# Performance work log

Measured on AMD Instinct MI355X. Metric: run time of the kernel, lower is better.

## Reference

```python
import jax, jax.numpy as jnp
import numpy as np

B, T, LD, PD, W, NL = 2048, 256, 32, 8, 64, 3
TH, CH = LD * 2, W * 2  # token/channel mixing hidden dims (expansion=2)


def setup_inputs() -> dict:
    key = jax.random.key(0)
    ks = jax.random.split(key, 12)
    n = lambda k, s, sc=0.02: jax.random.normal(k, s, jnp.float32) * sc
    return {
        "phys": jax.random.normal(ks[0], (B, T, PD), jnp.float32),
        "latents": jax.random.uniform(ks[1], (B, LD), jnp.float32),
        "pos_emb": n(ks[2], (1, LD, W)),
        "tokW": n(ks[3], (1, W)), "tokb": jnp.zeros((W,), jnp.float32),
        "physW1": n(ks[4], (PD, W)), "physb1": jnp.zeros((W,), jnp.float32),
        "physW2": n(ks[5], (W, W)), "physb2": jnp.zeros((W,), jnp.float32),
        "tn_g": jnp.ones((NL, W), jnp.float32), "tn_b": jnp.zeros((NL, W), jnp.float32),
        "tiW": n(ks[6], (NL, LD, TH)), "tib": jnp.zeros((NL, TH), jnp.float32),
        "toW": n(ks[7], (NL, TH, LD)), "tob": jnp.zeros((NL, LD), jnp.float32),
        "cn_g": jnp.ones((NL, W), jnp.float32), "cn_b": jnp.zeros((NL, W), jnp.float32),
        "ciW": n(ks[8], (NL, W, CH)), "cib": jnp.zeros((NL, CH), jnp.float32),
        "coW": n(ks[9], (NL, CH, W)), "cob": jnp.zeros((NL, W), jnp.float32),
        "hn_g": jnp.ones((W,), jnp.float32), "hn_b": jnp.zeros((W,), jnp.float32),
        "headW": n(ks[10], (W, 1), 0.0002),  # 0.02 init * 0.01 scaling from torch
        "headb": jnp.zeros((1,), jnp.float32),
    }


def _ln(x, g, b):
    m = jnp.mean(x, -1, keepdims=True)
    v = jnp.mean((x - m) ** 2, -1, keepdims=True)
    return (x - m) * jax.lax.rsqrt(v + 1e-5) * g + b


def reference(phys, latents, pos_emb, tokW, tokb, physW1, physb1, physW2, physb2,
              tn_g, tn_b, tiW, tib, toW, tob, cn_g, cn_b, ciW, cib, coW, cob,
              hn_g, hn_b, headW, headb):
    gelu = lambda x: jax.nn.gelu(x, approximate=False)  # torch nn.GELU default (exact)

    def step(current, phys_t):
        # token_projection of current[..., None]: Linear(1, W)
        tokens = current[:, :, None] * tokW[0] + tokb  # [B, LD, W]
        p = gelu(phys_t @ physW1 + physb1) @ physW2 + physb2  # [B, W]
        tokens = tokens + p[:, None, :] + pos_emb
        for i in range(NL):
            # token mixing: LN over width, mix across latent tokens
            mt = jnp.swapaxes(_ln(tokens, tn_g[i], tn_b[i]), 1, 2)  # [B, W, LD]
            mt = gelu(mt @ tiW[i] + tib[i]) @ toW[i] + tob[i]       # [B, W, LD]
            tokens = tokens + jnp.swapaxes(mt, 1, 2)
            # channel mixing over width
            mc = _ln(tokens, cn_g[i], cn_b[i])
            tokens = tokens + (gelu(mc @ ciW[i] + cib[i]) @ coW[i] + cob[i])
        delta = (_ln(tokens, hn_g, hn_b) @ headW + headb)[..., 0]  # [B, LD]
        new = jnp.clip(current + delta, 0.0, 1.0)
        return new, new

    _, outs = jax.lax.scan(step, latents, jnp.swapaxes(phys, 0, 1))  # [T, B, LD]
    return jnp.swapaxes(outs, 0, 1)  # [B, T, LD]
```

## Files before the change

### kernel.cpp

```cpp
#include <hip/hip_runtime.h>
#include <math.h>


namespace {
constexpr int Tt = 256, NL = 3;

typedef float    f32x4 __attribute__((ext_vector_type(4)));
typedef _Float16 half2 __attribute__((ext_vector_type(2)));
typedef _Float16 h16x4 __attribute__((ext_vector_type(4)));
typedef _Float16 h16x8 __attribute__((ext_vector_type(8)));

#define MFMA16(a, b, c) __builtin_amdgcn_mfma_f32_16x16x32_f16((a), (b), (c), 0, 0, 0)

__device__ __forceinline__ half2 h2c(float v) { return (half2)((_Float16)v); }
__device__ __forceinline__ f32x4 f4s(float v) { return (f32x4)v; }
__device__ __forceinline__ half2 pkrtz(float a, float b) {
    return __builtin_bit_cast(half2, __builtin_amdgcn_cvt_pkrtz(a, b));
}
__device__ __forceinline__ void st4h(short* p, half2 a, half2 b) {
    uint2 v;
    v.x = __builtin_bit_cast(unsigned int, a);
    v.y = __builtin_bit_cast(unsigned int, b);
    *(uint2*)p = v;
}
__device__ __forceinline__ half2 gelu_pk(half2 x) {
    half2 tc = __builtin_elementwise_min(__builtin_elementwise_max(x, h2c(-3.0f)), h2c(3.0f));
    half2 s = (tc * tc) * h2c(0.125f);
    half2 p = s * h2c(0.1455169f) + h2c(-0.446340f);
    p = s * p + h2c(0.604927f);
    p = s * p + h2c(-0.529702f);
    p = s * p + h2c(0.3989423f);
    return x * (h2c(0.5f) + tc * p);
}
__device__ __forceinline__ float gelu_f(float x) {
    float tc = fminf(fmaxf(x, -3.f), 3.f);
    float s = tc * tc;
    float p = fmaf(s, 3.55266e-5f, -8.71758e-4f);
    p = fmaf(s, p, 9.45198e-3f);
    p = fmaf(s, p, -6.62128e-2f);
    p = fmaf(s, p, 0.3989423f);
    return x * fmaf(tc, p, 0.5f);
}
__device__ __forceinline__ float rowsum16(float x) {
    x += __builtin_bit_cast(float, __builtin_amdgcn_update_dpp(0, __builtin_bit_cast(int, x), 0x121, 0xf, 0xf, false));
    x += __builtin_bit_cast(float, __builtin_amdgcn_update_dpp(0, __builtin_bit_cast(int, x), 0x122, 0xf, 0xf, false));
    x += __builtin_bit_cast(float, __builtin_amdgcn_update_dpp(0, __builtin_bit_cast(int, x), 0x124, 0xf, 0xf, false));
    x += __builtin_bit_cast(float, __builtin_amdgcn_update_dpp(0, __builtin_bit_cast(int, x), 0x128, 0xf, 0xf, false));
    return x;
}

__device__ __forceinline__ short f2h(float x) {
    return __builtin_bit_cast(short, (_Float16)x);
}

__global__ void lno_prep(const float* __restrict__ tiW, const float* __restrict__ toW,
                         const float* __restrict__ ciW, const float* __restrict__ coW,
                         const float* __restrict__ physW2, short* __restrict__ wsf) {
    int id = blockIdx.x * 256 + threadIdx.x;
    if (id < 6144) {
        int j = id & 7, lane = (id >> 3) & 63, g = id >> 9;
        int il = g >> 2, u = g & 3;
        int m = u * 16 + (lane & 15), k = (lane >> 4) * 8 + j;
        wsf[id] = f2h(tiW[il * 2048 + k * 64 + m]);
    } else if (id < 12288) {
        int t = id - 6144;
        int j = t & 7, lane = (t >> 3) & 63, g = t >> 9;
        int il = g >> 2, mt2 = (g >> 1) & 1, ks = g & 1;
        int m = mt2 * 16 + (lane & 15), k = ks * 32 + (lane >> 4) * 8 + j;
        wsf[id] = f2h(toW[il * 2048 + k * 32 + m]);
    } else if (id < 36864) {
        int t = id - 12288;
        int j = t & 7, lane = (t >> 3) & 63, g = t >> 9;
        int il = g >> 4, mtc = (g >> 1) & 7, ks = g & 1;
        int m = mtc * 16 + (lane & 15), k = ks * 32 + (lane >> 4) * 8 + j;
        wsf[id] = f2h(ciW[il * 8192 + k * 128 + m]);
    } else if (id < 61440) {
        int t = id - 36864;
        int j = t & 7, lane = (t >> 3) & 63, g = t >> 9;
        int il = g >> 4, nt = (g >> 2) & 3, ks = g & 3;
        int n = nt * 16 + (lane & 15), k = ks * 32 + (lane >> 4) * 8 + j;
        wsf[id] = f2h(coW[il * 8192 + k * 64 + n]);
    } else if (id < 65536) {
        int t = id - 61440;
        int w = t >> 6, k = t & 63;
        ((float*)(wsf + 61440))[t] = physW2[k * 64 + w];
    }
}

__global__ void lno_phys(const float* __restrict__ phys, const float* __restrict__ physW1,
                         const float* __restrict__ physb1, const float* __restrict__ physW2,
                         const float* __restrict__ physb2, short* __restrict__ pout) {
    __shared__ float hsh[4][64];
    const int lane = threadIdx.x & 63, wv = threadIdx.x >> 6;
    const size_t bt = (size_t)blockIdx.x * 4 + wv;
    const float* pt = phys + bt * 8;
    float4 px0 = *(const float4*)pt, px1 = *(const float4*)(pt + 4);
    float a = physb1[lane];
    a = fmaf(px0.x, physW1[0 * 64 + lane], a);
    a = fmaf(px0.y, physW1[1 * 64 + lane], a);
    a = fmaf(px0.z, physW1[2 * 64 + lane], a);
    a = fmaf(px0.w, physW1[3 * 64 + lane], a);
    a = fmaf(px1.x, physW1[4 * 64 + lane], a);
    a = fmaf(px1.y, physW1[5 * 64 + lane], a);
    a = fmaf(px1.z, physW1[6 * 64 + lane], a);
    a = fmaf(px1.w, physW1[7 * 64 + lane], a);
    hsh[wv][lane] = gelu_f(a);
    float acc = physb2[lane];
#pragma unroll
    for (int k = 0; k < 64; ++k) acc = fmaf(hsh[wv][k], physW2[k * 64 + lane], acc);
    pout[bt * 64 + (lane & 15) * 4 + (lane >> 4)] = f2h(acc);
}

__global__ __launch_bounds__(512, 2) void lno_scan(
    const float* __restrict__ latents, const float* __restrict__ pos_emb,
    const float* __restrict__ tokW,    const float* __restrict__ tokb,
    const float* __restrict__ tn_g,    const float* __restrict__ tn_b,
    const float* __restrict__ tib,     const float* __restrict__ tob,
    const float* __restrict__ cn_g,    const float* __restrict__ cn_b,
    const float* __restrict__ cib,     const float* __restrict__ cob,
    const float* __restrict__ hn_g,    const float* __restrict__ hn_b,
    const float* __restrict__ headW,   const float* __restrict__ headb,
    const short* __restrict__ wsf,     const short* pbuf, float* out)
{
    __shared__ __align__(16) short wAll[61440];
    __shared__ __align__(16) short scr[8][2048];
    __shared__ __align__(16) float biasL[1632];

    const int tid = threadIdx.x, lane = tid & 63, wv = tid >> 6;
    const int q = lane >> 4, c = lane & 15;
    const int b = blockIdx.x * 8 + wv;
    short* sc = scr[wv];

    const short* tiL = wAll;
    const short* toL = wAll + 6144;
    const short* ciL = wAll + 12288;
    const short* coL = wAll + 36864;

    {
        const unsigned int* src = (const unsigned int*)wsf;
#pragma unroll
        for (int i = 0; i < 15; ++i) {
            const int cid = wv * 15 + i;
            __builtin_amdgcn_global_load_lds(src + cid * 256 + lane * 4,
                                             (unsigned int*)&wAll[cid * 512], 16, 0, 0);
        }
    }
    for (int i = tid; i < 192; i += 512) {
        biasL[i] = tib[i];
        biasL[672 + i]  = tn_g[i];
        biasL[864 + i]  = tn_b[i];
        biasL[1056 + i] = cn_g[i];
        biasL[1248 + i] = cn_b[i];
        biasL[1440 + i] = cob[i];
    }
    for (int i = tid; i < 96;  i += 512) biasL[192 + i] = tob[i];
    for (int i = tid; i < 384; i += 512) biasL[288 + i] = cib[i];

    float tokw_r[4], tokb_r[4], gh_r[4];
#pragma unroll
    for (int nt = 0; nt < 4; ++nt) {
        tokw_r[nt] = tokW[nt * 16 + c];
        tokb_r[nt] = tokb[nt * 16 + c];
        gh_r[nt]   = hn_g[nt * 16 + c] * headW[nt * 16 + c];
    }
    float bhp = 0.f;
#pragma unroll
    for (int nt = 0; nt < 4; ++nt) bhp = fmaf(hn_b[nt * 16 + c], headW[nt * 16 + c], bhp);
    const float bh = rowsum16(bhp) + headb[0];

    f32x4 pe4[2][4];
#pragma unroll
    for (int mt = 0; mt < 2; ++mt)
#pragma unroll
        for (int nt = 0; nt < 4; ++nt)
#pragma unroll
            for (int r = 0; r < 4; ++r)
                pe4[mt][nt][r] = pos_emb[(mt * 16 + q * 4 + r) * 64 + nt * 16 + c];

    f32x4 cur8[2];
#pragma unroll
    for (int mt = 0; mt < 2; ++mt)
        cur8[mt] = *(const f32x4*)(latents + b * 32 + mt * 16 + q * 4);

    f32x4 tok[2][4];

    __syncthreads();

    auto stats = [&](f32x4 (&mean)[2], f32x4 (&rsig)[2]) {
#pragma unroll
        for (int mt = 0; mt < 2; ++mt) {
            f32x4 s4 = (tok[mt][0] + tok[mt][1]) + (tok[mt][2] + tok[mt][3]);
            f32x4 q4 = tok[mt][0] * tok[mt][0];
            q4 = __builtin_elementwise_fma(tok[mt][1], tok[mt][1], q4);
            q4 = __builtin_elementwise_fma(tok[mt][2], tok[mt][2], q4);
            q4 = __builtin_elementwise_fma(tok[mt][3], tok[mt][3], q4);
#pragma unroll
            for (int r = 0; r < 4; ++r) {
                float s = rowsum16(s4[r]);
                float qq = rowsum16(q4[r]);
                float m = s * 0.015625f;
                float v = fmaf(-m, m, qq * 0.015625f);
                mean[mt][r] = m;
                rsig[mt][r] = __builtin_amdgcn_rsqf(v + 1e-5f);
            }
        }
    };

    const short* pb = pbuf + (size_t)b * Tt * 64 + c * 4;
    h16x4 pvc = *(const h16x4*)pb;

#pragma unroll 1
    for (int t = 0; t < Tt; ++t) {
        const h16x4 pv = pvc;
        if (t + 1 < Tt) pvc = *(const h16x4*)(pb + (t + 1) * 64);

#pragma unroll
        for (int nt = 0; nt < 4; ++nt) {
            const f32x4 bp = f4s(tokb_r[nt] + (float)pv[nt]);
            const f32x4 tw = f4s(tokw_r[nt]);
#pragma unroll
            for (int mt = 0; mt < 2; ++mt)
                tok[mt][nt] = __builtin_elementwise_fma(cur8[mt], tw, pe4[mt][nt] + bp);
        }

#pragma unroll
        for (int il = 0; il < NL; ++il) {
            f32x4 mean[2], rsig[2];
            stats(mean, rsig);
            float tng[4], tnb[4];
#pragma unroll
            for (int nt = 0; nt < 4; ++nt) {
                tng[nt] = biasL[672 + il * 64 + nt * 16 + c];
                tnb[nt] = biasL[864 + il * 64 + nt * 16 + c];
            }
#pragma unroll
            for (int mt = 0; mt < 2; ++mt)
#pragma unroll
                for (int nt = 0; nt < 4; ++nt) {
                    f32x4 y = __builtin_elementwise_fma((tok[mt][nt] - mean[mt]) * rsig[mt],
                                                        f4s(tng[nt]), f4s(tnb[nt]));
                    st4h(&sc[(nt * 64 + (mt * 2 + (q >> 1)) * 16 + c) * 8 + (q & 1) * 4],
                         pkrtz(y[0], y[1]), pkrtz(y[2], y[3]));
                }
            h16x8 yfrag[4];
#pragma unroll
            for (int nt = 0; nt < 4; ++nt) yfrag[nt] = *(const h16x8*)&sc[(nt * 64 + lane) * 8];

#pragma unroll
            for (int mt = 0; mt < 2; ++mt) {
                const f32x4 tb = *(const f32x4*)&biasL[192 + il * 32 + mt * 16 + q * 4];
#pragma unroll
                for (int nt = 0; nt < 4; ++nt) tok[mt][nt] += tb;
            }
#pragma unroll
            for (int h = 0; h < 2; ++h) {
#pragma unroll
                for (int uu = 0; uu < 2; ++uu) {
                    const int u = h * 2 + uu;
                    const h16x8 a1 = *(const h16x8*)(tiL + ((il * 4 + u) * 64 + lane) * 8);
                    const f32x4 bi = *(const f32x4*)&biasL[il * 64 + u * 16 + q * 4];
#pragma unroll
                    for (int nt = 0; nt < 4; ++nt) {
                        f32x4 acc = MFMA16(a1, yfrag[nt], bi);
                        st4h(&sc[(nt * 64 + (uu * 2 + (q >> 1)) * 16 + c) * 8 + (q & 1) * 4],
                             gelu_pk(pkrtz(acc[0], acc[1])), gelu_pk(pkrtz(acc[2], acc[3])));
                    }
                }
                h16x8 hf[4];
#pragma unroll
                for (int nt = 0; nt < 4; ++nt) hf[nt] = *(const h16x8*)&sc[(nt * 64 + lane) * 8];
#pragma unroll
                for (int mt = 0; mt < 2; ++mt) {
                    const h16x8 a2 = *(const h16x8*)(toL + ((il * 4 + mt * 2 + h) * 64 + lane) * 8);
#pragma unroll
                    for (int nt = 0; nt < 4; ++nt) tok[mt][nt] = MFMA16(a2, hf[nt], tok[mt][nt]);
                }
            }

            stats(mean, rsig);
            float cng[4], cnb[4];
#pragma unroll
            for (int nt = 0; nt < 4; ++nt) {
                cng[nt] = biasL[1056 + il * 64 + nt * 16 + c];
                cnb[nt] = biasL[1248 + il * 64 + nt * 16 + c];
            }
#pragma unroll
            for (int mt = 0; mt < 2; ++mt)
#pragma unroll
                for (int nt = 0; nt < 4; ++nt) {
                    f32x4 v4 = __builtin_elementwise_fma((tok[mt][nt] - mean[mt]) * rsig[mt],
                                                         f4s(cng[nt]), f4s(cnb[nt]));
#pragma unroll
                    for (int r = 0; r < 4; ++r)
                        sc[(mt * 2 + (nt >> 1)) * 512 +
                           (q * 2 + (c >> 3) + 16 * r + 8 * (nt & 1)) * 8 + (c & 7)] = f2h(v4[r]);
                }
            h16x8 b3[4];
            {
                const int lp = ((c >> 2) * 2 + (q & 1)) + 8 * ((c & 3) * 2 + (q >> 1));
#pragma unroll
                for (int F = 0; F < 4; ++F) b3[F] = *(const h16x8*)&sc[F * 512 + lp * 8];
            }
#pragma unroll
            for (int nt = 0; nt < 4; ++nt) {
                const f32x4 cv = f4s(biasL[1440 + il * 64 + nt * 16 + c]);
#pragma unroll
                for (int mt = 0; mt < 2; ++mt) tok[mt][nt] += cv;
            }

#pragma unroll
            for (int hh = 0; hh < 2; ++hh) {
#pragma unroll
                for (int mm = 0; mm < 4; ++mm) {
                    const int mtc = hh * 4 + mm;
                    const h16x8 a30 = *(const h16x8*)(ciL + il * 8192 + (mtc * 2 + 0) * 512 + lane * 8);
                    const h16x8 a31 = *(const h16x8*)(ciL + il * 8192 + (mtc * 2 + 1) * 512 + lane * 8);
                    const f32x4 bi3 = *(const f32x4*)&biasL[288 + il * 128 + mtc * 16 + q * 4];
#pragma unroll
                    for (int ntl = 0; ntl < 2; ++ntl) {
                        f32x4 acc = MFMA16(a30, b3[ntl * 2 + 0], bi3);
                        acc = MFMA16(a31, b3[ntl * 2 + 1], acc);
                        st4h(&sc[((ntl * 2 + ((mtc >> 1) & 1)) * 64 +
                                  ((mtc & 1) * 2 + (q >> 1)) * 16 + c) * 8 + (q & 1) * 4],
                             gelu_pk(pkrtz(acc[0], acc[1])), gelu_pk(pkrtz(acc[2], acc[3])));
                    }
                }
                h16x8 a4[2][2];
#pragma unroll
                for (int mt = 0; mt < 2; ++mt)
#pragma unroll
                    for (int kk = 0; kk < 2; ++kk)
                        a4[mt][kk] = *(const h16x8*)&sc[((mt * 2 + kk) * 64 + lane) * 8];
#pragma unroll
                for (int nt = 0; nt < 4; ++nt) {
                    const h16x8 b40 = *(const h16x8*)(coL + il * 8192 + (nt * 4 + hh * 2 + 0) * 512 + lane * 8);
                    const h16x8 b41 = *(const h16x8*)(coL + il * 8192 + (nt * 4 + hh * 2 + 1) * 512 + lane * 8);
#pragma unroll
                    for (int mt = 0; mt < 2; ++mt) {
                        tok[mt][nt] = MFMA16(a4[mt][0], b40, tok[mt][nt]);
                        tok[mt][nt] = MFMA16(a4[mt][1], b41, tok[mt][nt]);
                    }
                }
            }
        }

        {
            f32x4 mean[2], rsig[2];
            stats(mean, rsig);
#pragma unroll
            for (int mt = 0; mt < 2; ++mt) {
                f32x4 l4 = (tok[mt][0] - mean[mt]) * f4s(gh_r[0]);
                l4 = __builtin_elementwise_fma(tok[mt][1] - mean[mt], f4s(gh_r[1]), l4);
                l4 = __builtin_elementwise_fma(tok[mt][2] - mean[mt], f4s(gh_r[2]), l4);
                l4 = __builtin_elementwise_fma(tok[mt][3] - mean[mt], f4s(gh_r[3]), l4);
                f32x4 ls;
#pragma unroll
                for (int r = 0; r < 4; ++r) ls[r] = rowsum16(l4[r]);
                f32x4 nv = cur8[mt] + __builtin_elementwise_fma(rsig[mt], ls, f4s(bh));
                nv = __builtin_elementwise_min(__builtin_elementwise_max(nv, f4s(0.f)), f4s(1.f));
                cur8[mt] = nv;
            }
            if (c == 0) {
                float* op = out + ((size_t)b * Tt + t) * 32 + q * 4;
                *(f32x4*)(op) = cur8[0];
                *(f32x4*)(op + 16) = cur8[1];
            }
        }
    }
}
}

extern "C" void kernel_launch(void* const* d_in, const int* in_sizes, int n_in,
                              void* d_out, int out_size, void* d_ws, size_t ws_size,
                              hipStream_t stream) {
    (void)in_sizes; (void)n_in; (void)ws_size; (void)out_size;
    const float* phys    = (const float*)d_in[0];
    const float* latents = (const float*)d_in[1];
    const float* pos_emb = (const float*)d_in[2];
    const float* tokW    = (const float*)d_in[3];
    const float* tokb    = (const float*)d_in[4];
    const float* physW1  = (const float*)d_in[5];
    const float* physb1  = (const float*)d_in[6];
    const float* physW2  = (const float*)d_in[7];
    const float* physb2  = (const float*)d_in[8];
    const float* tn_g    = (const float*)d_in[9];
    const float* tn_b    = (const float*)d_in[10];
    const float* tiW     = (const float*)d_in[11];
    const float* tib     = (const float*)d_in[12];
    const float* toW     = (const float*)d_in[13];
    const float* tob     = (const float*)d_in[14];
    const float* cn_g    = (const float*)d_in[15];
    const float* cn_b    = (const float*)d_in[16];
    const float* ciW     = (const float*)d_in[17];
    const float* cib     = (const float*)d_in[18];
    const float* coW     = (const float*)d_in[19];
    const float* cob     = (const float*)d_in[20];
    const float* hn_g    = (const float*)d_in[21];
    const float* hn_b    = (const float*)d_in[22];
    const float* headW   = (const float*)d_in[23];
    const float* headb   = (const float*)d_in[24];

    lno_prep<<<dim3(256), dim3(256), 0, stream>>>(tiW, toW, ciW, coW, physW2, (short*)d_ws);
    lno_phys<<<dim3(131072), dim3(256), 0, stream>>>(phys, physW1, physb1, physW2, physb2,
                                                     (short*)d_out);
    lno_scan<<<dim3(256), dim3(512), 0, stream>>>(
        latents, pos_emb, tokW, tokb, tn_g, tn_b, tib, tob,
        cn_g, cn_b, cib, cob, hn_g, hn_b, headW, headb,
        (const short*)d_ws, (const short*)d_out, (float*)d_out);
}
```

Measured before the change: 6.166 ms.

## Process two batch sequences per wavefront to add ILP in scan kernel

Each wavefront now carries two independent batch rows through the 256-step recurrence, so the block shrinks to 4 waves of 256 threads while keeping 8 rows per block. The two independent MFMA and LayerNorm chains are interleaved to hide latency on the serial time dependency, and weight A-fragments are reused across both rows. In exchange register pressure roughly doubles, the layer loop is no longer unrolled, and there are half as many waves per CU to hide stalls.

```diff
diff --git a/kernel.cpp b/kernel.cpp
--- a/kernel.cpp
+++ b/kernel.cpp
@@ -111,7 +111,7 @@
     pout[bt * 64 + (lane & 15) * 4 + (lane >> 4)] = f2h(acc);
 }
 
-__global__ __launch_bounds__(512, 2) void lno_scan(
+__global__ __launch_bounds__(256, 1) void lno_scan(
     const float* __restrict__ latents, const float* __restrict__ pos_emb,
     const float* __restrict__ tokW,    const float* __restrict__ tokb,
     const float* __restrict__ tn_g,    const float* __restrict__ tn_b,
@@ -123,29 +123,29 @@
     const short* __restrict__ wsf,     const short* pbuf, float* out)
 {
     __shared__ __align__(16) short wAll[61440];
-    __shared__ __align__(16) short scr[8][2048];
+    __shared__ __align__(16) short scr[4][4096];
     __shared__ __align__(16) float biasL[1632];
 
     const int tid = threadIdx.x, lane = tid & 63, wv = tid >> 6;
     const int q = lane >> 4, c = lane & 15;
-    const int b = blockIdx.x * 8 + wv;
-    short* sc = scr[wv];
+    const int bb = (blockIdx.x * 4 + wv) * 2;
 
     const short* tiL = wAll;
     const short* toL = wAll + 6144;
     const short* ciL = wAll + 12288;
     const short* coL = wAll + 36864;
+    short* const scp[2] = { &scr[wv][0], &scr[wv][2048] };
 
     {
         const unsigned int* src = (const unsigned int*)wsf;
 #pragma unroll
-        for (int i = 0; i < 15; ++i) {
-            const int cid = wv * 15 + i;
+        for (int i = 0; i < 30; ++i) {
+            const int cid = wv * 30 + i;
             __builtin_amdgcn_global_load_lds(src + cid * 256 + lane * 4,
                                              (unsigned int*)&wAll[cid * 512], 16, 0, 0);
         }
     }
-    for (int i = tid; i < 192; i += 512) {
+    for (int i = tid; i < 192; i += 256) {
         biasL[i] = tib[i];
         biasL[672 + i]  = tn_g[i];
         biasL[864 + i]  = tn_b[i];
@@ -153,8 +153,8 @@
         biasL[1248 + i] = cn_b[i];
         biasL[1440 + i] = cob[i];
     }
-    for (int i = tid; i < 96;  i += 512) biasL[192 + i] = tob[i];
-    for (int i = tid; i < 384; i += 512) biasL[288 + i] = cib[i];
+    for (int i = tid; i < 96;  i += 256) biasL[192 + i] = tob[i];
+    for (int i = tid; i < 384; i += 256) biasL[288 + i] = cib[i];
 
     float tokw_r[4], tokb_r[4], gh_r[4];
 #pragma unroll
@@ -177,28 +177,30 @@
             for (int r = 0; r < 4; ++r)
                 pe4[mt][nt][r] = pos_emb[(mt * 16 + q * 4 + r) * 64 + nt * 16 + c];
 
-    f32x4 cur8[2];
-#pragma unroll
-    for (int mt = 0; mt < 2; ++mt)
-        cur8[mt] = *(const f32x4*)(latents + b * 32 + mt * 16 + q * 4);
-
-    f32x4 tok[2][4];
+    f32x4 cur8[2][2];
+#pragma unroll
+    for (int s = 0; s < 2; ++s)
+#pragma unroll
+        for (int mt = 0; mt < 2; ++mt)
+            cur8[s][mt] = *(const f32x4*)(latents + (bb + s) * 32 + mt * 16 + q * 4);
+
+    f32x4 tok[2][2][4];
 
     __syncthreads();
 
-    auto stats = [&](f32x4 (&mean)[2], f32x4 (&rsig)[2]) {
+    auto stats1 = [&](const f32x4 (&tk)[2][4], f32x4 (&mean)[2], f32x4 (&rsig)[2]) {
 #pragma unroll
         for (int mt = 0; mt < 2; ++mt) {
-            f32x4 s4 = (tok[mt][0] + tok[mt][1]) + (tok[mt][2] + tok[mt][3]);
-            f32x4 q4 = tok[mt][0] * tok[mt][0];
-            q4 = __builtin_elementwise_fma(tok[mt][1], tok[mt][1], q4);
-            q4 = __builtin_elementwise_fma(tok[mt][2], tok[mt][2], q4);
-            q4 = __builtin_elementwise_fma(tok[mt][3], tok[mt][3], q4);
+            f32x4 s4 = (tk[mt][0] + tk[mt][1]) + (tk[mt][2] + tk[mt][3]);
+            f32x4 q4 = tk[mt][0] * tk[mt][0];
+            q4 = __builtin_elementwise_fma(tk[mt][1], tk[mt][1], q4);
+            q4 = __builtin_elementwise_fma(tk[mt][2], tk[mt][2], q4);
+            q4 = __builtin_elementwise_fma(tk[mt][3], tk[mt][3], q4);
 #pragma unroll
             for (int r = 0; r < 4; ++r) {
-                float s = rowsum16(s4[r]);
+                float ss = rowsum16(s4[r]);
                 float qq = rowsum16(q4[r]);
-                float m = s * 0.015625f;
+                float m = ss * 0.015625f;
                 float v = fmaf(-m, m, qq * 0.015625f);
                 mean[mt][r] = m;
                 rsig[mt][r] = __builtin_amdgcn_rsqf(v + 1e-5f);
@@ -206,27 +208,35 @@
         }
     };
 
-    const short* pb = pbuf + (size_t)b * Tt * 64 + c * 4;
-    h16x4 pvc = *(const h16x4*)pb;
+    const short* pb0 = pbuf + (size_t)(bb + 0) * Tt * 64 + c * 4;
+    const short* pb1 = pbuf + (size_t)(bb + 1) * Tt * 64 + c * 4;
+    h16x4 pvc0 = *(const h16x4*)pb0;
+    h16x4 pvc1 = *(const h16x4*)pb1;
 
 #pragma unroll 1
     for (int t = 0; t < Tt; ++t) {
-        const h16x4 pv = pvc;
-        if (t + 1 < Tt) pvc = *(const h16x4*)(pb + (t + 1) * 64);
-
-#pragma unroll
-        for (int nt = 0; nt < 4; ++nt) {
-            const f32x4 bp = f4s(tokb_r[nt] + (float)pv[nt]);
-            const f32x4 tw = f4s(tokw_r[nt]);
-#pragma unroll
-            for (int mt = 0; mt < 2; ++mt)
-                tok[mt][nt] = __builtin_elementwise_fma(cur8[mt], tw, pe4[mt][nt] + bp);
+        const h16x4 pv[2] = { pvc0, pvc1 };
+        if (t + 1 < Tt) {
+            pvc0 = *(const h16x4*)(pb0 + (t + 1) * 64);
+            pvc1 = *(const h16x4*)(pb1 + (t + 1) * 64);
         }
 
 #pragma unroll
+        for (int s = 0; s < 2; ++s)
+#pragma unroll
+            for (int nt = 0; nt < 4; ++nt) {
+                const f32x4 bp = f4s(tokb_r[nt] + (float)pv[s][nt]);
+                const f32x4 tw = f4s(tokw_r[nt]);
+#pragma unroll
+                for (int mt = 0; mt < 2; ++mt)
+                    tok[s][mt][nt] = __builtin_elementwise_fma(cur8[s][mt], tw, pe4[mt][nt] + bp);
+            }
+
+#pragma unroll 1
         for (int il = 0; il < NL; ++il) {
-            f32x4 mean[2], rsig[2];
-            stats(mean, rsig);
+            f32x4 mean[2][2], rsig[2][2];
+#pragma unroll
+            for (int s = 0; s < 2; ++s) stats1(tok[s], mean[s], rsig[s]);
             float tng[4], tnb[4];
 #pragma unroll
             for (int nt = 0; nt < 4; ++nt) {
@@ -234,50 +244,66 @@
                 tnb[nt] = biasL[864 + il * 64 + nt * 16 + c];
             }
 #pragma unroll
-            for (int mt = 0; mt < 2; ++mt)
-#pragma unroll
-                for (int nt = 0; nt < 4; ++nt) {
-                    f32x4 y = __builtin_elementwise_fma((tok[mt][nt] - mean[mt]) * rsig[mt],
-                                                        f4s(tng[nt]), f4s(tnb[nt]));
-                    st4h(&sc[(nt * 64 + (mt * 2 + (q >> 1)) * 16 + c) * 8 + (q & 1) * 4],
-                         pkrtz(y[0], y[1]), pkrtz(y[2], y[3]));
-                }
-            h16x8 yfrag[4];
-#pragma unroll
-            for (int nt = 0; nt < 4; ++nt) yfrag[nt] = *(const h16x8*)&sc[(nt * 64 + lane) * 8];
+            for (int s = 0; s < 2; ++s)
+#pragma unroll
+                for (int mt = 0; mt < 2; ++mt)
+#pragma unroll
+                    for (int nt = 0; nt < 4; ++nt) {
+                        f32x4 y = __builtin_elementwise_fma((tok[s][mt][nt] - mean[s][mt]) * rsig[s][mt],
+                                                            f4s(tng[nt]), f4s(tnb[nt]));
+                        st4h(&scp[s][(nt * 64 + (mt * 2 + (q >> 1)) * 16 + c) * 8 + (q & 1) * 4],
+                             pkrtz(y[0], y[1]), pkrtz(y[2], y[3]));
+                    }
+            h16x8 yfrag[2][4];
+#pragma unroll
+            for (int s = 0; s < 2; ++s)
+#pragma unroll
+                for (int nt = 0; nt < 4; ++nt)
+                    yfrag[s][nt] = *(const h16x8*)&scp[s][(nt * 64 + lane) * 8];
 
 #pragma unroll
             for (int mt = 0; mt < 2; ++mt) {
                 const f32x4 tb = *(const f32x4*)&biasL[192 + il * 32 + mt * 16 + q * 4];
 #pragma unroll
-                for (int nt = 0; nt < 4; ++nt) tok[mt][nt] += tb;
+                for (int s = 0; s < 2; ++s)
+#pragma unroll
+                    for (int nt = 0; nt < 4; ++nt) tok[s][mt][nt] += tb;
             }
 #pragma unroll
             for (int h = 0; h < 2; ++h) {
 #pragma unroll
                 for (int uu = 0; uu < 2; ++uu) {
-                    const int u = h * 2 + uu;
-                    const h16x8 a1 = *(const h16x8*)(tiL + ((il * 4 + u) * 64 + lane) * 8);
-                    const f32x4 bi = *(const f32x4*)&biasL[il * 64 + u * 16 + q * 4];
-#pragma unroll
-                    for (int nt = 0; nt < 4; ++nt) {
-                        f32x4 acc = MFMA16(a1, yfrag[nt], bi);
-                        st4h(&sc[(nt * 64 + (uu * 2 + (q >> 1)) * 16 + c) * 8 + (q & 1) * 4],
-                             gelu_pk(pkrtz(acc[0], acc[1])), gelu_pk(pkrtz(acc[2], acc[3])));
-                    }
-                }
-                h16x8 hf[4];
-#pragma unroll
-                for (int nt = 0; nt < 4; ++nt) hf[nt] = *(const h16x8*)&sc[(nt * 64 + lane) * 8];
+                    const int uw = h * 2 + uu;
+                    const h16x8 a1 = *(const h16x8*)(tiL + ((il * 4 + uw) * 64 + lane) * 8);
+                    const f32x4 bi = *(const f32x4*)&biasL[il * 64 + uw * 16 + q * 4];
+#pragma unroll
+                    for (int s = 0; s < 2; ++s)
+#pragma unroll
+                        for (int nt = 0; nt < 4; ++nt) {
+                            f32x4 acc = MFMA16(a1, yfrag[s][nt], bi);
+                            st4h(&scp[s][(nt * 64 + (uu * 2 + (q >> 1)) * 16 + c) * 8 + (q & 1) * 4],
+                                 gelu_pk(pkrtz(acc[0], acc[1])), gelu_pk(pkrtz(acc[2], acc[3])));
+                        }
+                }
+                h16x8 hf[2][4];
+#pragma unroll
+                for (int s = 0; s < 2; ++s)
+#pragma unroll
+                    for (int nt = 0; nt < 4; ++nt)
+                        hf[s][nt] = *(const h16x8*)&scp[s][(nt * 64 + lane) * 8];
 #pragma unroll
                 for (int mt = 0; mt < 2; ++mt) {
                     const h16x8 a2 = *(const h16x8*)(toL + ((il * 4 + mt * 2 + h) * 64 + lane) * 8);
 #pragma unroll
-                    for (int nt = 0; nt < 4; ++nt) tok[mt][nt] = MFMA16(a2, hf[nt], tok[mt][nt]);
-                }
-            }
-
-            stats(mean, rsig);
+                    for (int s = 0; s < 2; ++s)
+#pragma unroll
+                        for (int nt = 0; nt < 4; ++nt)
+                            tok[s][mt][nt] = MFMA16(a2, hf[s][nt], tok[s][mt][nt]);
+                }
+            }
+
+#pragma unroll
+            for (int s = 0; s < 2; ++s) stats1(tok[s], mean[s], rsig[s]);
             float cng[4], cnb[4];
 #pragma unroll
             for (int nt = 0; nt < 4; ++nt) {
@@ -285,27 +311,34 @@
                 cnb[nt] = biasL[1248 + il * 64 + nt * 16 + c];
             }
 #pragma unroll
-            for (int mt = 0; mt < 2; ++mt)
-#pragma unroll
-                for (int nt = 0; nt < 4; ++nt) {
-                    f32x4 v4 = __builtin_elementwise_fma((tok[mt][nt] - mean[mt]) * rsig[mt],
-                                                         f4s(cng[nt]), f4s(cnb[nt]));
-#pragma unroll
-                    for (int r = 0; r < 4; ++r)
-                        sc[(mt * 2 + (nt >> 1)) * 512 +
-                           (q * 2 + (c >> 3) + 16 * r + 8 * (nt & 1)) * 8 + (c & 7)] = f2h(v4[r]);
-                }
-            h16x8 b3[4];
+            for (int s = 0; s < 2; ++s)
+#pragma unroll
+                for (int mt = 0; mt < 2; ++mt)
+#pragma unroll
+                    for (int nt = 0; nt < 4; ++nt) {
+                        f32x4 v4 = __builtin_elementwise_fma((tok[s][mt][nt] - mean[s][mt]) * rsig[s][mt],
+                                                             f4s(cng[nt]), f4s(cnb[nt]));
+#pragma unroll
+                        for (int r = 0; r < 4; ++r)
+                            scp[s][(mt * 2 + (nt >> 1)) * 512 +
+                                   (q * 2 + (c >> 3) + 16 * r + 8 * (nt & 1)) * 8 + (c & 7)] = f2h(v4[r]);
+                    }
+            h16x8 b3[2][4];
             {
                 const int lp = ((c >> 2) * 2 + (q & 1)) + 8 * ((c & 3) * 2 + (q >> 1));
 #pragma unroll
-                for (int F = 0; F < 4; ++F) b3[F] = *(const h16x8*)&sc[F * 512 + lp * 8];
+                for (int s = 0; s < 2; ++s)
+#pragma unroll
+                    for (int F = 0; F < 4; ++F)
+                        b3[s][F] = *(const h16x8*)&scp[s][F * 512 + lp * 8];
             }
 #pragma unroll
             for (int nt = 0; nt < 4; ++nt) {
                 const f32x4 cv = f4s(biasL[1440 + il * 64 + nt * 16 + c]);
 #pragma unroll
-                for (int mt = 0; mt < 2; ++mt) tok[mt][nt] += cv;
+                for (int s = 0; s < 2; ++s)
+#pragma unroll
+                    for (int mt = 0; mt < 2; ++mt) tok[s][mt][nt] += cv;
             }
 
 #pragma unroll
@@ -317,53 +350,65 @@
                     const h16x8 a31 = *(const h16x8*)(ciL + il * 8192 + (mtc * 2 + 1) * 512 + lane * 8);
                     const f32x4 bi3 = *(const f32x4*)&biasL[288 + il * 128 + mtc * 16 + q * 4];
 #pragma unroll
-                    for (int ntl = 0; ntl < 2; ++ntl) {
-                        f32x4 acc = MFMA16(a30, b3[ntl * 2 + 0], bi3);
-                        acc = MFMA16(a31, b3[ntl * 2 + 1], acc);
-                        st4h(&sc[((ntl * 2 + ((mtc >> 1) & 1)) * 64 +
-                                  ((mtc & 1) * 2 + (q >> 1)) * 16 + c) * 8 + (q & 1) * 4],
-                             gelu_pk(pkrtz(acc[0], acc[1])), gelu_pk(pkrtz(acc[2], acc[3])));
-                    }
-                }
-                h16x8 a4[2][2];
-#pragma unroll
-                for (int mt = 0; mt < 2; ++mt)
-#pragma unroll
-                    for (int kk = 0; kk < 2; ++kk)
-                        a4[mt][kk] = *(const h16x8*)&sc[((mt * 2 + kk) * 64 + lane) * 8];
+                    for (int s = 0; s < 2; ++s)
+#pragma unroll
+                        for (int ntl = 0; ntl < 2; ++ntl) {
+                            f32x4 acc = MFMA16(a30, b3[s][ntl * 2 + 0], bi3);
+                            acc = MFMA16(a31, b3[s][ntl * 2 + 1], acc);
+                            st4h(&scp[s][((ntl * 2 + ((mtc >> 1) & 1)) * 64 +
+                                          ((mtc & 1) * 2 + (q >> 1)) * 16 + c) * 8 + (q & 1) * 4],
+                                 gelu_pk(pkrtz(acc[0], acc[1])), gelu_pk(pkrtz(acc[2], acc[3])));
+                        }
+                }
+                h16x8 a4[2][2][2];
+#pragma unroll
+                for (int s = 0; s < 2; ++s)
+#pragma unroll
+                    for (int mt = 0; mt < 2; ++mt)
+#pragma unroll
+                        for (int kk = 0; kk < 2; ++kk)
+                            a4[s][mt][kk] = *(const h16x8*)&scp[s][((mt * 2 + kk) * 64 + lane) * 8];
 #pragma unroll
                 for (int nt = 0; nt < 4; ++nt) {
                     const h16x8 b40 = *(const h16x8*)(coL + il * 8192 + (nt * 4 + hh * 2 + 0) * 512 + lane * 8);
                     const h16x8 b41 = *(const h16x8*)(coL + il * 8192 + (nt * 4 + hh * 2 + 1) * 512 + lane * 8);
 #pragma unroll
-                    for (int mt = 0; mt < 2; ++mt) {
-                        tok[mt][nt] = MFMA16(a4[mt][0], b40, tok[mt][nt]);
-                        tok[mt][nt] = MFMA16(a4[mt][1], b41, tok[mt][nt]);
-                    }
+                    for (int s = 0; s < 2; ++s)
+#pragma unroll
+                        for (int mt = 0; mt < 2; ++mt) {
+                            tok[s][mt][nt] = MFMA16(a4[s][mt][0], b40, tok[s][mt][nt]);
+                            tok[s][mt][nt] = MFMA16(a4[s][mt][1], b41, tok[s][mt][nt]);
+                        }
                 }
             }
         }
 
         {
-            f32x4 mean[2], rsig[2];
-            stats(mean, rsig);
-#pragma unroll
-            for (int mt = 0; mt < 2; ++mt) {
-                f32x4 l4 = (tok[mt][0] - mean[mt]) * f4s(gh_r[0]);
-                l4 = __builtin_elementwise_fma(tok[mt][1] - mean[mt], f4s(gh_r[1]), l4);
-                l4 = __builtin_elementwise_fma(tok[mt][2] - mean[mt], f4s(gh_r[2]), l4);
-                l4 = __builtin_elementwise_fma(tok[mt][3] - mean[mt], f4s(gh_r[3]), l4);
-                f32x4 ls;
-#pragma unroll
-                for (int r = 0; r < 4; ++r) ls[r] = rowsum16(l4[r]);
-                f32x4 nv = cur8[mt] + __builtin_elementwise_fma(rsig[mt], ls, f4s(bh));
-                nv = __builtin_elementwise_min(__builtin_elementwise_max(nv, f4s(0.f)), f4s(1.f));
-                cur8[mt] = nv;
-            }
+            f32x4 mean[2][2], rsig[2][2];
+#pragma unroll
+            for (int s = 0; s < 2; ++s) stats1(tok[s], mean[s], rsig[s]);
+#pragma unroll
+            for (int s = 0; s < 2; ++s)
+#pragma unroll
+                for (int mt = 0; mt < 2; ++mt) {
+                    f32x4 l4 = (tok[s][mt][0] - mean[s][mt]) * f4s(gh_r[0]);
+                    l4 = __builtin_elementwise_fma(tok[s][mt][1] - mean[s][mt], f4s(gh_r[1]), l4);
+                    l4 = __builtin_elementwise_fma(tok[s][mt][2] - mean[s][mt], f4s(gh_r[2]), l4);
+                    l4 = __builtin_elementwise_fma(tok[s][mt][3] - mean[s][mt], f4s(gh_r[3]), l4);
+                    f32x4 ls;
+#pragma unroll
+                    for (int r = 0; r < 4; ++r) ls[r] = rowsum16(l4[r]);
+                    f32x4 nv = cur8[s][mt] + __builtin_elementwise_fma(rsig[s][mt], ls, f4s(bh));
+                    nv = __builtin_elementwise_min(__builtin_elementwise_max(nv, f4s(0.f)), f4s(1.f));
+                    cur8[s][mt] = nv;
+                }
             if (c == 0) {
-                float* op = out + ((size_t)b * Tt + t) * 32 + q * 4;
-                *(f32x4*)(op) = cur8[0];
-                *(f32x4*)(op + 16) = cur8[1];
+#pragma unroll
+                for (int s = 0; s < 2; ++s) {
+                    float* op = out + ((size_t)(bb + s) * Tt + t) * 32 + q * 4;
+                    *(f32x4*)(op) = cur8[s][0];
+                    *(f32x4*)(op + 16) = cur8[s][1];
+                }
             }
         }
     }
@@ -403,7 +448,7 @@
     lno_prep<<<dim3(256), dim3(256), 0, stream>>>(tiW, toW, ciW, coW, physW2, (short*)d_ws);
     lno_phys<<<dim3(131072), dim3(256), 0, stream>>>(phys, physW1, physb1, physW2, physb2,
                                                      (short*)d_out);
-    lno_scan<<<dim3(256), dim3(512), 0, stream>>>(
+    lno_scan<<<dim3(256), dim3(256), 0, stream>>>(
         latents, pos_emb, tokW, tokb, tn_g, tn_b, tib, tob,
         cn_g, cn_b, cib, cob, hn_g, hn_b, headW, headb,
         (const short*)d_ws, (const short*)d_out, (float*)d_out);
```

Result: slower. 8.026 ms (+30.2%).

## Use 16x16x16 MFMA for token mixing to keep fragments in registers

Applied to the files above, without the earlier changes.

Token mixing now uses the K=16 MFMA variant, whose accumulator layout matches its B-operand layout, so LN outputs and GELU hidden activations pass between MFMAs directly in registers instead of round-tripping through LDS scratch. The weight pre-pack for tiW/toW is changed to the 4-element fragment layout, and pos_emb plus tokb are folded and stored as fp16 registers. Launch bounds are relaxed to one block per SM, giving more registers per thread at the cost of occupancy. The extra register pressure from holding b2[4][4] may cause spills or lower latency hiding.

```diff
diff --git a/kernel.cpp b/kernel.cpp
--- a/kernel.cpp
+++ b/kernel.cpp
@@ -10,7 +10,8 @@
 typedef _Float16 h16x4 __attribute__((ext_vector_type(4)));
 typedef _Float16 h16x8 __attribute__((ext_vector_type(8)));
 
-#define MFMA16(a, b, c) __builtin_amdgcn_mfma_f32_16x16x32_f16((a), (b), (c), 0, 0, 0)
+#define MFMA32(a, b, c) __builtin_amdgcn_mfma_f32_16x16x32_f16((a), (b), (c), 0, 0, 0)
+#define MFMA16(a, b, c) __builtin_amdgcn_mfma_f32_16x16x16f16((a), (b), (c), 0, 0, 0)
 
 __device__ __forceinline__ half2 h2c(float v) { return (half2)((_Float16)v); }
 __device__ __forceinline__ f32x4 f4s(float v) { return (f32x4)v; }
@@ -22,6 +23,9 @@
     v.x = __builtin_bit_cast(unsigned int, a);
     v.y = __builtin_bit_cast(unsigned int, b);
     *(uint2*)p = v;
+}
+__device__ __forceinline__ h16x4 h4(half2 a, half2 b) {
+    h16x4 v; v[0] = a[0]; v[1] = a[1]; v[2] = b[0]; v[3] = b[1]; return v;
 }
 __device__ __forceinline__ half2 gelu_pk(half2 x) {
     half2 tc = __builtin_elementwise_min(__builtin_elementwise_max(x, h2c(-3.0f)), h2c(3.0f));
@@ -48,7 +52,6 @@
     x += __builtin_bit_cast(float, __builtin_amdgcn_update_dpp(0, __builtin_bit_cast(int, x), 0x128, 0xf, 0xf, false));
     return x;
 }
-
 __device__ __forceinline__ short f2h(float x) {
     return __builtin_bit_cast(short, (_Float16)x);
 }
@@ -58,16 +61,18 @@
                          const float* __restrict__ physW2, short* __restrict__ wsf) {
     int id = blockIdx.x * 256 + threadIdx.x;
     if (id < 6144) {
-        int j = id & 7, lane = (id >> 3) & 63, g = id >> 9;
-        int il = g >> 2, u = g & 3;
-        int m = u * 16 + (lane & 15), k = (lane >> 4) * 8 + j;
-        wsf[id] = f2h(tiW[il * 2048 + k * 64 + m]);
+        int e = id & 255, tile = id >> 8;
+        int lane = e >> 2, j = e & 3;
+        int q = lane >> 4, cc = lane & 15;
+        int kc = tile & 1, u = (tile >> 1) & 3, il = tile >> 3;
+        wsf[id] = f2h(tiW[il * 2048 + (16 * kc + 4 * q + j) * 64 + 16 * u + cc]);
     } else if (id < 12288) {
         int t = id - 6144;
-        int j = t & 7, lane = (t >> 3) & 63, g = t >> 9;
-        int il = g >> 2, mt2 = (g >> 1) & 1, ks = g & 1;
-        int m = mt2 * 16 + (lane & 15), k = ks * 32 + (lane >> 4) * 8 + j;
-        wsf[id] = f2h(toW[il * 2048 + k * 32 + m]);
+        int e = t & 255, tile = t >> 8;
+        int lane = e >> 2, j = e & 3;
+        int q = lane >> 4, cc = lane & 15;
+        int kc = tile & 3, mt = (tile >> 2) & 1, il = tile >> 3;
+        wsf[id] = f2h(toW[il * 2048 + (16 * kc + 4 * q + j) * 32 + 16 * mt + cc]);
     } else if (id < 36864) {
         int t = id - 12288;
         int j = t & 7, lane = (t >> 3) & 63, g = t >> 9;
@@ -111,7 +116,7 @@
     pout[bt * 64 + (lane & 15) * 4 + (lane >> 4)] = f2h(acc);
 }
 
-__global__ __launch_bounds__(512, 2) void lno_scan(
+__global__ __launch_bounds__(512, 1) void lno_scan(
     const float* __restrict__ latents, const float* __restrict__ pos_emb,
     const float* __restrict__ tokW,    const float* __restrict__ tokb,
     const float* __restrict__ tn_g,    const float* __restrict__ tn_b,
@@ -131,10 +136,10 @@
     const int b = blockIdx.x * 8 + wv;
     short* sc = scr[wv];
 
-    const short* tiL = wAll;
-    const short* toL = wAll + 6144;
-    const short* ciL = wAll + 12288;
-    const short* coL = wAll + 36864;
+    const short* A1L = wAll;
+    const short* A2L = wAll + 6144;
+    const short* A3L = wAll + 12288;
+    const short* B4L = wAll + 36864;
 
     {
         const unsigned int* src = (const unsigned int*)wsf;
@@ -156,11 +161,10 @@
     for (int i = tid; i < 96;  i += 512) biasL[192 + i] = tob[i];
     for (int i = tid; i < 384; i += 512) biasL[288 + i] = cib[i];
 
-    float tokw_r[4], tokb_r[4], gh_r[4];
+    float tokw_r[4], gh_r[4];
 #pragma unroll
     for (int nt = 0; nt < 4; ++nt) {
         tokw_r[nt] = tokW[nt * 16 + c];
-        tokb_r[nt] = tokb[nt * 16 + c];
         gh_r[nt]   = hn_g[nt * 16 + c] * headW[nt * 16 + c];
     }
     float bhp = 0.f;
@@ -168,14 +172,18 @@
     for (int nt = 0; nt < 4; ++nt) bhp = fmaf(hn_b[nt * 16 + c], headW[nt * 16 + c], bhp);
     const float bh = rowsum16(bhp) + headb[0];
 
-    f32x4 pe4[2][4];
+    h16x4 peh[2][4];
 #pragma unroll
     for (int mt = 0; mt < 2; ++mt)
 #pragma unroll
-        for (int nt = 0; nt < 4; ++nt)
-#pragma unroll
-            for (int r = 0; r < 4; ++r)
-                pe4[mt][nt][r] = pos_emb[(mt * 16 + q * 4 + r) * 64 + nt * 16 + c];
+        for (int r = 0; r < 4; ++r) {
+            const int row = mt * 16 + q * 4 + r;
+            float v0 = pos_emb[row * 64 +  0 + c] + tokb[ 0 + c];
+            float v1 = pos_emb[row * 64 + 16 + c] + tokb[16 + c];
+            float v2 = pos_emb[row * 64 + 32 + c] + tokb[32 + c];
+            float v3 = pos_emb[row * 64 + 48 + c] + tokb[48 + c];
+            peh[mt][r] = h4(pkrtz(v0, v1), pkrtz(v2, v3));
+        }
 
     f32x4 cur8[2];
 #pragma unroll
@@ -196,9 +204,9 @@
             q4 = __builtin_elementwise_fma(tok[mt][3], tok[mt][3], q4);
 #pragma unroll
             for (int r = 0; r < 4; ++r) {
-                float s = rowsum16(s4[r]);
+                float ss = rowsum16(s4[r]);
                 float qq = rowsum16(q4[r]);
-                float m = s * 0.015625f;
+                float m = ss * 0.015625f;
                 float v = fmaf(-m, m, qq * 0.015625f);
                 mean[mt][r] = m;
                 rsig[mt][r] = __builtin_amdgcn_rsqf(v + 1e-5f);
@@ -214,68 +222,75 @@
         const h16x4 pv = pvc;
         if (t + 1 < Tt) pvc = *(const h16x4*)(pb + (t + 1) * 64);
 
-#pragma unroll
-        for (int nt = 0; nt < 4; ++nt) {
-            const f32x4 bp = f4s(tokb_r[nt] + (float)pv[nt]);
-            const f32x4 tw = f4s(tokw_r[nt]);
+        {
+            f32x4 pvx;
+#pragma unroll
+            for (int nt = 0; nt < 4; ++nt) pvx[nt] = (float)pv[nt];
 #pragma unroll
             for (int mt = 0; mt < 2; ++mt)
-                tok[mt][nt] = __builtin_elementwise_fma(cur8[mt], tw, pe4[mt][nt] + bp);
+#pragma unroll
+                for (int r = 0; r < 4; ++r) {
+#pragma unroll
+                    for (int nt = 0; nt < 4; ++nt)
+                        tok[nt == 0 ? mt : mt][nt][r] =
+                            0.f;
+                }
+#pragma unroll
+            for (int mt = 0; mt < 2; ++mt)
+#pragma unroll
+                for (int r = 0; r < 4; ++r) {
+#pragma unroll
+                    for (int nt = 0; nt < 4; ++nt)
+                        tok[mt][nt][r] = fmaf(cur8[mt][r], tokw_r[nt],
+                                              (float)peh[mt][r][nt] + pvx[nt]);
+                }
         }
 
 #pragma unroll
         for (int il = 0; il < NL; ++il) {
             f32x4 mean[2], rsig[2];
             stats(mean, rsig);
-            float tng[4], tnb[4];
+            h16x4 yh[2][4];
 #pragma unroll
             for (int nt = 0; nt < 4; ++nt) {
-                tng[nt] = biasL[672 + il * 64 + nt * 16 + c];
-                tnb[nt] = biasL[864 + il * 64 + nt * 16 + c];
-            }
-#pragma unroll
-            for (int mt = 0; mt < 2; ++mt)
-#pragma unroll
-                for (int nt = 0; nt < 4; ++nt) {
+                const float tng = biasL[672 + il * 64 + nt * 16 + c];
+                const float tnb = biasL[864 + il * 64 + nt * 16 + c];
+#pragma unroll
+                for (int mt = 0; mt < 2; ++mt) {
                     f32x4 y = __builtin_elementwise_fma((tok[mt][nt] - mean[mt]) * rsig[mt],
-                                                        f4s(tng[nt]), f4s(tnb[nt]));
-                    st4h(&sc[(nt * 64 + (mt * 2 + (q >> 1)) * 16 + c) * 8 + (q & 1) * 4],
-                         pkrtz(y[0], y[1]), pkrtz(y[2], y[3]));
-                }
-            h16x8 yfrag[4];
-#pragma unroll
-            for (int nt = 0; nt < 4; ++nt) yfrag[nt] = *(const h16x8*)&sc[(nt * 64 + lane) * 8];
-
+                                                        f4s(tng), f4s(tnb));
+                    yh[mt][nt] = h4(pkrtz(y[0], y[1]), pkrtz(y[2], y[3]));
+                }
+            }
 #pragma unroll
             for (int mt = 0; mt < 2; ++mt) {
                 const f32x4 tb = *(const f32x4*)&biasL[192 + il * 32 + mt * 16 + q * 4];
 #pragma unroll
                 for (int nt = 0; nt < 4; ++nt) tok[mt][nt] += tb;
             }
-#pragma unroll
-            for (int h = 0; h < 2; ++h) {
-#pragma unroll
-                for (int uu = 0; uu < 2; ++uu) {
-                    const int u = h * 2 + uu;
-                    const h16x8 a1 = *(const h16x8*)(tiL + ((il * 4 + u) * 64 + lane) * 8);
-                    const f32x4 bi = *(const f32x4*)&biasL[il * 64 + u * 16 + q * 4];
-#pragma unroll
-                    for (int nt = 0; nt < 4; ++nt) {
-                        f32x4 acc = MFMA16(a1, yfrag[nt], bi);
-                        st4h(&sc[(nt * 64 + (uu * 2 + (q >> 1)) * 16 + c) * 8 + (q & 1) * 4],
-                             gelu_pk(pkrtz(acc[0], acc[1])), gelu_pk(pkrtz(acc[2], acc[3])));
-                    }
-                }
-                h16x8 hf[4];
-#pragma unroll
-                for (int nt = 0; nt < 4; ++nt) hf[nt] = *(const h16x8*)&sc[(nt * 64 + lane) * 8];
-#pragma unroll
-                for (int mt = 0; mt < 2; ++mt) {
-                    const h16x8 a2 = *(const h16x8*)(toL + ((il * 4 + mt * 2 + h) * 64 + lane) * 8);
-#pragma unroll
-                    for (int nt = 0; nt < 4; ++nt) tok[mt][nt] = MFMA16(a2, hf[nt], tok[mt][nt]);
-                }
-            }
+            h16x4 b2[4][4];
+#pragma unroll
+            for (int u = 0; u < 4; ++u) {
+                const h16x4 a1k0 = *(const h16x4*)(A1L + ((il * 4 + u) * 2 + 0) * 256 + lane * 4);
+                const h16x4 a1k1 = *(const h16x4*)(A1L + ((il * 4 + u) * 2 + 1) * 256 + lane * 4);
+                const f32x4 bi = *(const f32x4*)&biasL[il * 64 + u * 16 + q * 4];
+#pragma unroll
+                for (int nt = 0; nt < 4; ++nt) {
+                    f32x4 hv = MFMA16(a1k0, yh[0][nt], bi);
+                    hv = MFMA16(a1k1, yh[1][nt], hv);
+                    b2[u][nt] = h4(gelu_pk(pkrtz(hv[0], hv[1])),
+                                   gelu_pk(pkrtz(hv[2], hv[3])));
+                }
+            }
+#pragma unroll
+            for (int mt = 0; mt < 2; ++mt)
+#pragma unroll
+                for (int kc = 0; kc < 4; ++kc) {
+                    const h16x4 a2 = *(const h16x4*)(A2L + ((il * 2 + mt) * 4 + kc) * 256 + lane * 4);
+#pragma unroll
+                    for (int nt = 0; nt < 4; ++nt)
+                        tok[mt][nt] = MFMA16(a2, b2[kc][nt], tok[mt][nt]);
+                }
 
             stats(mean, rsig);
             float cng[4], cnb[4];
@@ -307,19 +322,18 @@
 #pragma unroll
                 for (int mt = 0; mt < 2; ++mt) tok[mt][nt] += cv;
             }
-
 #pragma unroll
             for (int hh = 0; hh < 2; ++hh) {
 #pragma unroll
                 for (int mm = 0; mm < 4; ++mm) {
                     const int mtc = hh * 4 + mm;
-                    const h16x8 a30 = *(const h16x8*)(ciL + il * 8192 + (mtc * 2 + 0) * 512 + lane * 8);
-                    const h16x8 a31 = *(const h16x8*)(ciL + il * 8192 + (mtc * 2 + 1) * 512 + lane * 8);
+                    const h16x8 a30 = *(const h16x8*)(A3L + il * 8192 + (mtc * 2 + 0) * 512 + lane * 8);
+                    const h16x8 a31 = *(const h16x8*)(A3L + il * 8192 + (mtc * 2 + 1) * 512 + lane * 8);
                     const f32x4 bi3 = *(const f32x4*)&biasL[288 + il * 128 + mtc * 16 + q * 4];
 #pragma unroll
                     for (int ntl = 0; ntl < 2; ++ntl) {
-                        f32x4 acc = MFMA16(a30, b3[ntl * 2 + 0], bi3);
-                        acc = MFMA16(a31, b3[ntl * 2 + 1], acc);
+                        f32x4 acc = MFMA32(a30, b3[ntl * 2 + 0], bi3);
+                        acc = MFMA32(a31, b3[ntl * 2 + 1], acc);
                         st4h(&sc[((ntl * 2 + ((mtc >> 1) & 1)) * 64 +
                                   ((mtc & 1) * 2 + (q >> 1)) * 16 + c) * 8 + (q & 1) * 4],
                              gelu_pk(pkrtz(acc[0], acc[1])), gelu_pk(pkrtz(acc[2], acc[3])));
@@ -333,12 +347,12 @@
                         a4[mt][kk] = *(const h16x8*)&sc[((mt * 2 + kk) * 64 + lane) * 8];
 #pragma unroll
                 for (int nt = 0; nt < 4; ++nt) {
-                    const h16x8 b40 = *(const h16x8*)(coL + il * 8192 + (nt * 4 + hh * 2 + 0) * 512 + lane * 8);
-                    const h16x8 b41 = *(const h16x8*)(coL + il * 8192 + (nt * 4 + hh * 2 + 1) * 512 + lane * 8);
+                    const h16x8 b40 = *(const h16x8*)(B4L + il * 8192 + (nt * 4 + hh * 2 + 0) * 512 + lane * 8);
+                    const h16x8 b41 = *(const h16x8*)(B4L + il * 8192 + (nt * 4 + hh * 2 + 1) * 512 + lane * 8);
 #pragma unroll
                     for (int mt = 0; mt < 2; ++mt) {
-                        tok[mt][nt] = MFMA16(a4[mt][0], b40, tok[mt][nt]);
-                        tok[mt][nt] = MFMA16(a4[mt][1], b41, tok[mt][nt]);
+                        tok[mt][nt] = MFMA32(a4[mt][0], b40, tok[mt][nt]);
+                        tok[mt][nt] = MFMA32(a4[mt][1], b41, tok[mt][nt]);
                     }
                 }
             }
```

Measured after the change: 6.059 ms. About the same (-1.7%).
